# Kernel tuning notes

Hardware: AMD Instinct MI355X
Metric: run time of the kernel (lower is better)

Reference implementation:

```python
import jax, jax.numpy as jnp
import numpy as np
from jax import lax

H = 32  # hidden_size


def setup_inputs() -> dict:
    key = jax.random.key(0)
    ks = jax.random.split(key, 8)
    B, T, I, O = 64, 16384, 1, 1
    s_ih = 1.0 / np.sqrt(H)
    inp = {
        "x": jax.random.normal(ks[0], (B, T, I), dtype=jnp.float32),
        # PyTorch nn.LSTM params: weight_ih_l0 [4H, I], weight_hh_l0 [4H, H], biases [4H]
        "W_ih": jax.random.uniform(ks[1], (4 * H, I), dtype=jnp.float32, minval=-s_ih, maxval=s_ih),
        "W_hh": jax.random.uniform(ks[2], (4 * H, H), dtype=jnp.float32, minval=-s_ih, maxval=s_ih),
        "b_ih": jax.random.uniform(ks[3], (4 * H,), dtype=jnp.float32, minval=-s_ih, maxval=s_ih),
        "b_hh": jax.random.uniform(ks[4], (4 * H,), dtype=jnp.float32, minval=-s_ih, maxval=s_ih),
        # Linear(H, O)
        "W_lin": jax.random.uniform(ks[5], (O, H), dtype=jnp.float32, minval=-s_ih, maxval=s_ih),
        "b_lin": jax.random.uniform(ks[6], (O,), dtype=jnp.float32, minval=-s_ih, maxval=s_ih),
    }
    return inp


def _lstm_seq(x, W_ih, W_hh, b_ih, b_hh):
    """Single-layer LSTM over (B, T, I) -> hidden sequence (B, T, H).
    PyTorch gate order: i, f, g, o."""
    B, T, _ = x.shape
    # Precompute input contribution for all timesteps: (B, T, 4H)
    xg = jnp.einsum("bti,gi->btg", x, W_ih) + (b_ih + b_hh)

    W_hh_T = W_hh.T  # (H, 4H)

    def step(carry, xg_t):
        h, c = carry  # each (B, H)
        gates = xg_t + h @ W_hh_T  # (B, 4H)
        i, f, g, o = jnp.split(gates, 4, axis=-1)
        i = jax.nn.sigmoid(i)
        f = jax.nn.sigmoid(f)
        g = jnp.tanh(g)
        o = jax.nn.sigmoid(o)
        c = f * c + i * g
        h = o * jnp.tanh(c)
        return (h, c), h

    h0 = jnp.zeros((B, H), dtype=x.dtype)
    c0 = jnp.zeros((B, H), dtype=x.dtype)
    _, hs = lax.scan(step, (h0, c0), jnp.swapaxes(xg, 0, 1))  # hs: (T, B, H)
    return jnp.swapaxes(hs, 0, 1)  # (B, T, H)


def reference(x, W_ih, W_hh, b_ih, b_hh, W_lin, b_lin):
    hs = _lstm_seq(x, W_ih, W_hh, b_ih, b_hh)  # (B, T, H)
    linear_out = jnp.einsum("bth,oh->bto", hs, W_lin) + b_lin  # (B, T, O)
    return x + linear_out  # residual skip connection
```

## Files before the change

kernel.cpp:

```cpp
#include <hip/hip_runtime.h>


#define HID 32
#define CHUNK 32

typedef float f2 __attribute__((ext_vector_type(2)));
typedef float f4 __attribute__((ext_vector_type(4)));

__device__ __forceinline__ float rl(float v, int lane) {
    return __int_as_float(__builtin_amdgcn_readlane(__float_as_int(v), lane));
}

__device__ __forceinline__ float fsig(float v) {
    float e = __builtin_amdgcn_exp2f(v * -1.44269504088896340736f);
    return __builtin_amdgcn_rcpf(1.0f + e);
}
__device__ __forceinline__ float ftanh(float v) {
    float e = __builtin_amdgcn_exp2f(v * -2.88539008177792681472f);
    float r = __builtin_amdgcn_rcpf(1.0f + e);
    return __builtin_fmaf(2.0f, r, -1.0f);
}

__global__ __launch_bounds__(64, 1)
void lstm_wave_scan(const float* __restrict__ x,
                    const float* __restrict__ W_ih,
                    const float* __restrict__ W_hh,
                    const float* __restrict__ b_ih,
                    const float* __restrict__ b_hh,
                    const float* __restrict__ W_lin,
                    const float* __restrict__ b_lin,
                    float* __restrict__ out,
                    int T) {
    __shared__ float h_hist[CHUNK][65];

    const int lane = threadIdx.x;
    const int j    = lane & 31;
    const int half = lane >> 5;
    const int b    = blockIdx.x;

    const int row1 = j + (half << 5);
    const int row2 = 64 + j + (half << 5);

    f2 w1[16], w2[16];
    {
        const f4* R1 = (const f4*)(W_hh + row1 * HID);
        const f4* R2 = (const f4*)(W_hh + row2 * HID);
#pragma unroll
        for (int m = 0; m < 8; ++m) {
            f4 v;
            v = R1[m]; w1[2*m] = {v.x, v.y}; w1[2*m+1] = {v.z, v.w};
            v = R2[m]; w2[2*m] = {v.x, v.y}; w2[2*m+1] = {v.z, v.w};
        }
    }
    const float wih1 = W_ih[row1], bb1 = b_ih[row1] + b_hh[row1];
    const float wih2 = W_ih[row2], bb2 = b_ih[row2] + b_hh[row2];

    const float pa = half ? -1.44269504088896340736f : -2.88539008177792681472f;
    const float pb = half ? 1.0f : 2.0f;
    const float pc = half ? 0.0f : -1.0f;

    const float blin = b_lin[0];

    float c = 0.0f;
    f2 hp[16];
#pragma unroll
    for (int k = 0; k < 16; ++k) hp[k] = {0.0f, 0.0f};

    const float* xb = x   + (size_t)b * T;
    float*       ob = out + (size_t)b * T;

    float xv = xb[j];

    for (int t0 = 0; t0 < T; t0 += CHUNK) {
        int t0n = t0 + CHUNK; if (t0n >= T) t0n = 0;
        float xv_next = xb[t0n + j];

#pragma unroll 4
        for (int tt = 0; tt < CHUNK; ++tt) {
            const float sx = rl(xv, tt);

            f2 acc1 = { __builtin_fmaf(sx, wih1, bb1), 0.0f };
            f2 acc2 = { __builtin_fmaf(sx, wih2, bb2), 0.0f };
#pragma unroll
            for (int m = 0; m < 16; ++m) {
                acc1 = __builtin_elementwise_fma(w1[m], hp[m], acc1);
                acc2 = __builtin_elementwise_fma(w2[m], hp[m], acc2);
            }
            const float g1 = acc1.x + acc1.y;
            const float g2 = acc2.x + acc2.y;

            const float a1 = fsig(g1);
            const float e2 = __builtin_amdgcn_exp2f(g2 * pa);
            const float a2 = __builtin_fmaf(pb, __builtin_amdgcn_rcpf(1.0f + e2), pc);

            const float p = a1 * a2;
            const float q = __shfl_xor(p, 32, 64);

            c = __builtin_fmaf(a1, c, q);
            const float h = a2 * ftanh(c);

            h_hist[tt][lane] = h;

#pragma unroll
            for (int k = 0; k < 16; ++k)
                hp[k] = { rl(h, 32 + 2*k), rl(h, 32 + 2*k + 1) };
        }

        {
            float facc = 0.0f;
#pragma unroll
            for (int k = 0; k < 32; ++k)
                facc = __builtin_fmaf(W_lin[k], h_hist[j][32 + k], facc);
            if (half == 0)
                ob[t0 + j] = xv + facc + blin;
        }

        xv = xv_next;
    }
}

extern "C" void kernel_launch(void* const* d_in, const int* in_sizes, int n_in,
                              void* d_out, int out_size, void* d_ws, size_t ws_size,
                              hipStream_t stream) {
    const float* x     = (const float*)d_in[0];
    const float* W_ih  = (const float*)d_in[1];
    const float* W_hh  = (const float*)d_in[2];
    const float* b_ih  = (const float*)d_in[3];
    const float* b_hh  = (const float*)d_in[4];
    const float* W_lin = (const float*)d_in[5];
    const float* b_lin = (const float*)d_in[6];
    float* out = (float*)d_out;

    const int B = 64;
    const int T = in_sizes[0] / B;

    dim3 grid(B);
    dim3 block(64);
    lstm_wave_scan<<<grid, block, 0, stream>>>(x, W_ih, W_hh, b_ih, b_hh,
                                               W_lin, b_lin, out, T);
}
```

Baseline: 3.573 ms.

## Process two batch elements per wave with four gates per lane via bpermute

Restructures the wave so each 32-lane half runs an independent batch sequence, each lane computing all four gates for one hidden unit and halving the grid. The h broadcast switches from scalar readlanes to ds_bpermute, and gate weights and biases are pre-scaled by the exp2 constants to drop multiplies in the activations. This removes the cross-half shuffle per step but doubles the per-lane FMA chain and adds LDS permute latency to the serial recurrence.

```diff
diff --git a/kernel.cpp b/kernel.cpp
--- a/kernel.cpp
+++ b/kernel.cpp
@@ -7,22 +7,12 @@
 typedef float f2 __attribute__((ext_vector_type(2)));
 typedef float f4 __attribute__((ext_vector_type(4)));
 
-__device__ __forceinline__ float rl(float v, int lane) {
-    return __int_as_float(__builtin_amdgcn_readlane(__float_as_int(v), lane));
-}
-
-__device__ __forceinline__ float fsig(float v) {
-    float e = __builtin_amdgcn_exp2f(v * -1.44269504088896340736f);
-    return __builtin_amdgcn_rcpf(1.0f + e);
-}
-__device__ __forceinline__ float ftanh(float v) {
-    float e = __builtin_amdgcn_exp2f(v * -2.88539008177792681472f);
-    float r = __builtin_amdgcn_rcpf(1.0f + e);
-    return __builtin_fmaf(2.0f, r, -1.0f);
+__device__ __forceinline__ float bperm(int byte_addr, float v) {
+    return __int_as_float(__builtin_amdgcn_ds_bpermute(byte_addr, __float_as_int(v)));
 }
 
 __global__ __launch_bounds__(64, 1)
-void lstm_wave_scan(const float* __restrict__ x,
+void lstm_pair_scan(const float* __restrict__ x,
                     const float* __restrict__ W_ih,
                     const float* __restrict__ W_hh,
                     const float* __restrict__ b_ih,
@@ -36,35 +26,36 @@
     const int lane = threadIdx.x;
     const int j    = lane & 31;
     const int half = lane >> 5;
-    const int b    = blockIdx.x;
+    const int b    = (blockIdx.x << 1) + half;
 
-    const int row1 = j + (half << 5);
-    const int row2 = 64 + j + (half << 5);
+    const float S1 = -1.44269504088896340736f;
+    const float S2 = -2.88539008177792681472f;
 
-    f2 w1[16], w2[16];
+    f2 wi[16], wf[16], wg[16], wo[16];
     {
-        const f4* R1 = (const f4*)(W_hh + row1 * HID);
-        const f4* R2 = (const f4*)(W_hh + row2 * HID);
+        const f4* Ri = (const f4*)(W_hh + (0  + j) * HID);
+        const f4* Rf = (const f4*)(W_hh + (32 + j) * HID);
+        const f4* Rg = (const f4*)(W_hh + (64 + j) * HID);
+        const f4* Ro = (const f4*)(W_hh + (96 + j) * HID);
 #pragma unroll
         for (int m = 0; m < 8; ++m) {
             f4 v;
-            v = R1[m]; w1[2*m] = {v.x, v.y}; w1[2*m+1] = {v.z, v.w};
-            v = R2[m]; w2[2*m] = {v.x, v.y}; w2[2*m+1] = {v.z, v.w};
+            v = Ri[m]; wi[2*m] = {v.x*S1, v.y*S1}; wi[2*m+1] = {v.z*S1, v.w*S1};
+            v = Rf[m]; wf[2*m] = {v.x*S1, v.y*S1}; wf[2*m+1] = {v.z*S1, v.w*S1};
+            v = Rg[m]; wg[2*m] = {v.x*S2, v.y*S2}; wg[2*m+1] = {v.z*S2, v.w*S2};
+            v = Ro[m]; wo[2*m] = {v.x*S1, v.y*S1}; wo[2*m+1] = {v.z*S1, v.w*S1};
         }
     }
-    const float wih1 = W_ih[row1], bb1 = b_ih[row1] + b_hh[row1];
-    const float wih2 = W_ih[row2], bb2 = b_ih[row2] + b_hh[row2];
+    const float wih_i = W_ih[j]      * S1, bi = (b_ih[j]      + b_hh[j])      * S1;
+    const float wih_f = W_ih[32 + j] * S1, bf = (b_ih[32 + j] + b_hh[32 + j]) * S1;
+    const float wih_g = W_ih[64 + j] * S2, bg = (b_ih[64 + j] + b_hh[64 + j]) * S2;
+    const float wih_o = W_ih[96 + j] * S1, bo = (b_ih[96 + j] + b_hh[96 + j]) * S1;
+    const float blin  = b_lin[0];
 
-    const float pa = half ? -1.44269504088896340736f : -2.88539008177792681472f;
-    const float pb = half ? 1.0f : 2.0f;
-    const float pc = half ? 0.0f : -1.0f;
-
-    const float blin = b_lin[0];
+    const int vbase = half << 7;
 
     float c = 0.0f;
-    f2 hp[16];
-#pragma unroll
-    for (int k = 0; k < 16; ++k) hp[k] = {0.0f, 0.0f};
+    float h = 0.0f;
 
     const float* xb = x   + (size_t)b * T;
     float*       ob = out + (size_t)b * T;
@@ -77,42 +68,44 @@
 
 #pragma unroll 4
         for (int tt = 0; tt < CHUNK; ++tt) {
-            const float sx = rl(xv, tt);
+            const float xk = bperm(vbase + 4 * tt, xv);
 
-            f2 acc1 = { __builtin_fmaf(sx, wih1, bb1), 0.0f };
-            f2 acc2 = { __builtin_fmaf(sx, wih2, bb2), 0.0f };
+            f2 ai = {bi, 0.0f}, af2 = {bf, 0.0f}, ag = {bg, 0.0f}, ao = {bo, 0.0f};
 #pragma unroll
             for (int m = 0; m < 16; ++m) {
-                acc1 = __builtin_elementwise_fma(w1[m], hp[m], acc1);
-                acc2 = __builtin_elementwise_fma(w2[m], hp[m], acc2);
+                const float h0 = bperm(vbase + 8 * m,     h);
+                const float h1 = bperm(vbase + 8 * m + 4, h);
+                const f2 hm = {h0, h1};
+                ai  = __builtin_elementwise_fma(wi[m], hm, ai);
+                af2 = __builtin_elementwise_fma(wf[m], hm, af2);
+                ag  = __builtin_elementwise_fma(wg[m], hm, ag);
+                ao  = __builtin_elementwise_fma(wo[m], hm, ao);
             }
-            const float g1 = acc1.x + acc1.y;
-            const float g2 = acc2.x + acc2.y;
+            const float gi = __builtin_fmaf(xk, wih_i, ai.x  + ai.y);
+            const float gf = __builtin_fmaf(xk, wih_f, af2.x + af2.y);
+            const float gg = __builtin_fmaf(xk, wih_g, ag.x  + ag.y);
+            const float go = __builtin_fmaf(xk, wih_o, ao.x  + ao.y);
 
-            const float a1 = fsig(g1);
-            const float e2 = __builtin_amdgcn_exp2f(g2 * pa);
-            const float a2 = __builtin_fmaf(pb, __builtin_amdgcn_rcpf(1.0f + e2), pc);
+            const float ii = __builtin_amdgcn_rcpf(1.0f + __builtin_amdgcn_exp2f(gi));
+            const float ff = __builtin_amdgcn_rcpf(1.0f + __builtin_amdgcn_exp2f(gf));
+            const float g_ = __builtin_fmaf(2.0f,
+                               __builtin_amdgcn_rcpf(1.0f + __builtin_amdgcn_exp2f(gg)), -1.0f);
+            const float oo = __builtin_amdgcn_rcpf(1.0f + __builtin_amdgcn_exp2f(go));
 
-            const float p = a1 * a2;
-            const float q = __shfl_xor(p, 32, 64);
-
-            c = __builtin_fmaf(a1, c, q);
-            const float h = a2 * ftanh(c);
+            c = __builtin_fmaf(ff, c, ii * g_);
+            const float th = __builtin_fmaf(2.0f,
+                               __builtin_amdgcn_rcpf(1.0f + __builtin_amdgcn_exp2f(c * S2)), -1.0f);
+            h = oo * th;
 
             h_hist[tt][lane] = h;
-
-#pragma unroll
-            for (int k = 0; k < 16; ++k)
-                hp[k] = { rl(h, 32 + 2*k), rl(h, 32 + 2*k + 1) };
         }
 
         {
             float facc = 0.0f;
 #pragma unroll
             for (int k = 0; k < 32; ++k)
-                facc = __builtin_fmaf(W_lin[k], h_hist[j][32 + k], facc);
-            if (half == 0)
-                ob[t0 + j] = xv + facc + blin;
+                facc = __builtin_fmaf(W_lin[k], h_hist[j][(half << 5) + k], facc);
+            ob[t0 + j] = xv + facc + blin;
         }
 
         xv = xv_next;
@@ -134,8 +127,8 @@
     const int B = 64;
     const int T = in_sizes[0] / B;
 
-    dim3 grid(B);
+    dim3 grid(B / 2);
     dim3 block(64);
-    lstm_wave_scan<<<grid, block, 0, stream>>>(x, W_ih, W_hh, b_ih, b_hh,
+    lstm_pair_scan<<<grid, block, 0, stream>>>(x, W_ih, W_hh, b_ih, b_hh,
                                                W_lin, b_lin, out, T);
 }
```

After: 6.685 ms. +87.1%, slower.
